# Kernel optimization log

Measured on AMD Instinct MI355X. Metric: run time of the kernel, lower is better.

Reference implementation:

```python
import jax, jax.numpy as jnp
import numpy as np


def setup_inputs() -> dict:
    key = jax.random.key(0)
    ks = jax.random.split(key, 4)
    d, d_k, d_v = 1024, 128, 128
    B, S = 4, 4096
    scale = 1.0 / np.sqrt(d)
    return {
        "X": jax.random.normal(ks[0], (B, S, d), dtype=jnp.float32),
        "W_q": jax.random.normal(ks[1], (d, d_k), dtype=jnp.float32) * scale,
        "b_q": jnp.zeros((d_k,), dtype=jnp.float32),
        "W_k": jax.random.normal(ks[2], (d, d_k), dtype=jnp.float32) * scale,
        "b_k": jnp.zeros((d_k,), dtype=jnp.float32),
        "W_v": jax.random.normal(ks[3], (d, d_v), dtype=jnp.float32) * scale,
        "b_v": jnp.zeros((d_v,), dtype=jnp.float32),
    }


def reference(X, W_q, b_q, W_k, b_k, W_v, b_v):
    # Projections: [B, S, d_k/d_v]
    Q = jnp.einsum("bsd,dk->bsk", X, W_q) + b_q
    K = jnp.einsum("bsd,dk->bsk", X, W_k) + b_k
    V = jnp.einsum("bsd,dv->bsv", X, W_v) + b_v

    d_k = Q.shape[-1]
    # Scaled dot-product scores: [B, S, S]
    scores = jnp.einsum("bqk,bsk->bqs", Q, K) / jnp.sqrt(jnp.float32(d_k))
    # Causal (lower-triangular) mask
    S = scores.shape[-1]
    causal = jnp.tril(jnp.ones((S, S), dtype=bool))
    scores = jnp.where(causal[None, :, :], scores, -jnp.inf)
    weights = jax.nn.softmax(scores, axis=-1)
    # Weighted sum of values: [B, S, d_v]
    return jnp.einsum("bqs,bsv->bqv", weights, V)
```

## Files before the change

### kernel.cpp

```cpp
#include <hip/hip_runtime.h>
#include <hip/hip_bf16.h>
#include <stdint.h>


typedef __bf16 bf16x8 __attribute__((ext_vector_type(8)));
typedef float  f32x4  __attribute__((ext_vector_type(4)));
typedef unsigned int u32x4 __attribute__((ext_vector_type(4)));
typedef unsigned int u32x2 __attribute__((ext_vector_type(2)));

using bf16 = __hip_bfloat16;

#define AS1 __attribute__((address_space(1)))
#define AS3 __attribute__((address_space(3)))

__device__ __forceinline__ void gl_lds16(const void* g, void* l) {
  __builtin_amdgcn_global_load_lds((AS1 uint32_t*)g, (AS3 uint32_t*)l, 16, 0, 0);
}

__global__ __launch_bounds__(256) void k_wt(const float* __restrict__ Wq,
                                            const float* __restrict__ Wk,
                                            const float* __restrict__ Wv,
                                            bf16* __restrict__ Wt) {
  __shared__ bf16 t[64][72];
  const float* W = blockIdx.z == 0 ? Wq : (blockIdx.z == 1 ? Wk : Wv);
  int k0 = blockIdx.x * 64, n0 = blockIdx.y * 64;
  int tid = threadIdx.x;
  int r = tid >> 4, c4 = (tid & 15) * 4;
#pragma unroll
  for (int s = 0; s < 4; ++s) {
    int rr = r + s * 16;
    float4 v = *(const float4*)(W + (size_t)(k0 + rr) * 128 + n0 + c4);
    t[rr][c4 + 0] = __float2bfloat16(v.x);
    t[rr][c4 + 1] = __float2bfloat16(v.y);
    t[rr][c4 + 2] = __float2bfloat16(v.z);
    t[rr][c4 + 3] = __float2bfloat16(v.w);
  }
  __syncthreads();
  bf16* out = Wt + (size_t)blockIdx.z * 128 * 1024;
#pragma unroll
  for (int s = 0; s < 4; ++s) {
    int rn = r + s * 16;
    union { bf16 h[4]; u32x2 v; } u;
    u.h[0] = t[c4 + 0][rn]; u.h[1] = t[c4 + 1][rn];
    u.h[2] = t[c4 + 2][rn]; u.h[3] = t[c4 + 3][rn];
    *(u32x2*)(out + (size_t)(n0 + rn) * 1024 + k0 + c4) = u.v;
  }
}

__global__ __launch_bounds__(512) void k_qkv(const float* __restrict__ X,
                                             const bf16* __restrict__ Wt,
                                             const float* __restrict__ bq,
                                             const float* __restrict__ bk,
                                             const float* __restrict__ bv,
                                             bf16* __restrict__ Qo,
                                             bf16* __restrict__ Ko,
                                             bf16* __restrict__ Vt) {
  __shared__ __align__(16) char smem[65536];
  float* Xs = (float*)smem;
  bf16* Ws = (bf16*)(smem + 16384);
  bf16* Vs = (bf16*)smem;

  const int m0 = blockIdx.x * 64;
  const int tid = threadIdx.x;
  const int lane = tid & 63;
  const int li = lane & 15, g = lane >> 4;
  const int wid = tid >> 6;
  const int wm = wid >> 2, wn = wid & 3;

  const int xr = tid >> 3;
  const int xc32 = (tid & 7) >> 1;
  const int xhf = tid & 1;
  const int wr = tid >> 2;
  const int wc = tid & 3;

  f32x4 acc[3][2][2] = {};

  {
    gl_lds16(X + (size_t)(m0 + xr) * 1024 + (xc32 ^ (xr & 3)) * 8 + xhf * 4,
             Xs + tid * 4);
#pragma unroll
    for (int z = 0; z < 3; ++z)
      gl_lds16(Wt + (size_t)z * 131072 + (size_t)wr * 1024 + (wc ^ (wr & 3)) * 8,
               Ws + z * 4096 + tid * 8);
  }
  int cur = 0;
  for (int kt = 0; kt < 32; ++kt) {
    __syncthreads();
    if (kt < 31) {
      const int k0 = (kt + 1) * 32;
      gl_lds16(X + (size_t)(m0 + xr) * 1024 + k0 + (xc32 ^ (xr & 3)) * 8 + xhf * 4,
               Xs + (cur ^ 1) * 2048 + tid * 4);
#pragma unroll
      for (int z = 0; z < 3; ++z)
        gl_lds16(Wt + (size_t)z * 131072 + (size_t)wr * 1024 + k0 + (wc ^ (wr & 3)) * 8,
                 Ws + (cur ^ 1) * 12288 + z * 4096 + tid * 8);
    }
    bf16x8 af[2];
#pragma unroll
    for (int mf = 0; mf < 2; ++mf) {
      int r = wm * 32 + mf * 16 + li;
      const float* xp = Xs + cur * 2048 + r * 32 + ((g ^ (r & 3)) * 8);
      f32x4 x0 = *(const f32x4*)xp;
      f32x4 x1 = *(const f32x4*)(xp + 4);
      union { bf16 h[8]; bf16x8 v; } u;
      u.h[0] = __float2bfloat16(x0[0]); u.h[1] = __float2bfloat16(x0[1]);
      u.h[2] = __float2bfloat16(x0[2]); u.h[3] = __float2bfloat16(x0[3]);
      u.h[4] = __float2bfloat16(x1[0]); u.h[5] = __float2bfloat16(x1[1]);
      u.h[6] = __float2bfloat16(x1[2]); u.h[7] = __float2bfloat16(x1[3]);
      af[mf] = u.v;
    }
#pragma unroll
    for (int z = 0; z < 3; ++z) {
#pragma unroll
      for (int nf = 0; nf < 2; ++nf) {
        int r = wn * 32 + nf * 16 + li;
        bf16x8 bfrag =
            *(const bf16x8*)(Ws + cur * 12288 + z * 4096 + r * 32 + ((g ^ (r & 3)) * 8));
#pragma unroll
        for (int mf = 0; mf < 2; ++mf)
          acc[z][mf][nf] = __builtin_amdgcn_mfma_f32_16x16x32_bf16(
              af[mf], bfrag, acc[z][mf][nf], 0, 0, 0);
      }
    }
    cur ^= 1;
  }

#pragma unroll
  for (int z = 0; z < 2; ++z) {
    const float* bias = z == 0 ? bq : bk;
    bf16* Out = z == 0 ? Qo : Ko;
    const float scale = z == 0 ? 0.12752404368678202f : 1.0f;
#pragma unroll
    for (int nf = 0; nf < 2; ++nf) {
      int col = wn * 32 + nf * 16 + li;
      float bb = bias[col];
#pragma unroll
      for (int mf = 0; mf < 2; ++mf)
#pragma unroll
        for (int j = 0; j < 4; ++j) {
          int row = m0 + wm * 32 + mf * 16 + g * 4 + j;
          Out[(size_t)row * 128 + col] =
              __float2bfloat16((acc[z][mf][nf][j] + bb) * scale);
        }
    }
  }

  __syncthreads();
#pragma unroll
  for (int nf = 0; nf < 2; ++nf) {
    int col = wn * 32 + nf * 16 + li;
    float bb = bv[col];
#pragma unroll
    for (int mf = 0; mf < 2; ++mf)
#pragma unroll
      for (int j = 0; j < 4; ++j) {
        int row = wm * 32 + mf * 16 + g * 4 + j;
        Vs[row * 136 + col] = __float2bfloat16(acc[2][mf][nf][j] + bb);
      }
  }
  __syncthreads();
  const int b = m0 >> 12;
  const int s_off = m0 & 4095;
#pragma unroll
  for (int t2 = 0; t2 < 2; ++t2) {
    int idx = tid + 512 * t2;
    int dv = idx & 127;
    int sg = idx >> 7;
    union { bf16 h[8]; u32x4 v; } u;
#pragma unroll
    for (int si = 0; si < 8; ++si) u.h[si] = Vs[(sg * 8 + si) * 136 + dv];
    *(u32x4*)(Vt + (size_t)(b * 128 + dv) * 4096 + s_off + sg * 8) = u.v;
  }
}

__global__ __launch_bounds__(512, 4) void k_attn(const bf16* __restrict__ Qb,
                                                 const bf16* __restrict__ Kb,
                                                 const bf16* __restrict__ Vt,
                                                 bf16* __restrict__ o_part,
                                                 float* __restrict__ l_part) {
  __shared__ __align__(16) bf16 Kls[2][64 * 128];
  __shared__ __align__(16) bf16 Vls[2][128 * 64];
  __shared__ __align__(16) bf16 Pls[8][16 * 36];

  const int bid = blockIdx.x;
  const int xcd = bid & 7;
  const int slot = xcd * 72 + (bid >> 3);
  const int b = slot / 144;
  const int s = 143 - (slot - b * 144);
  const int widx = b * 144 + s;
  int qt = 0;
#pragma unroll
  for (int q2 = 1; q2 < 32; ++q2) {
    int M = q2 >> 2;
    if ((M + 1) * (2 * M + (q2 & 3)) <= s) qt = q2;
  }
  const int Mq = qt >> 2;
  const int chunk = s - (Mq + 1) * (2 * Mq + (qt & 3));
  const int ntiles = 2 * qt + 2;
  const int nch = (qt + 4) >> 2;
  const int clen = ntiles / nch;
  const int crem = ntiles - clen * nch;
  const int kt0 = chunk * clen + min(chunk, crem);
  const int kt1 = kt0 + clen + (chunk < crem ? 1 : 0) - 1;

  const int tid = threadIdx.x;
  const int lane = tid & 63;
  const int li = lane & 15, g = lane >> 4;
  const int w8 = tid >> 6;

  bf16x8 qf[4];
#pragma unroll
  for (int ks = 0; ks < 4; ++ks)
    qf[ks] = *(const bf16x8*)(Qb +
        (size_t)(b * 4096 + qt * 128 + w8 * 16 + li) * 128 + ks * 32 + g * 8);

  f32x4 o[8] = {};
  f32x4 lacc = {};
  bf16x8 ones;
#pragma unroll
  for (int e = 0; e < 8; ++e) ones[e] = (__bf16)1.0f;

  bf16* P = &Pls[w8][0];
  const bf16* Vtb = Vt + (size_t)b * 128 * 4096;

  {
    const int kv0 = kt0 * 64;
#pragma unroll
    for (int ii = 0; ii < 2; ++ii) {
      int c = tid + 512 * ii;
      int r = c >> 4, cc = c & 15;
      gl_lds16(Kb + (size_t)(b * 4096 + kv0 + r) * 128 + (cc ^ (r & 7)) * 8,
               &Kls[0][c * 8]);
      int r2 = c >> 3, cc2 = c & 7;
      gl_lds16(Vtb + (size_t)r2 * 4096 + kv0 + (cc2 ^ (r2 & 7)) * 8,
               &Vls[0][c * 8]);
    }
  }
  int cur = 0;
  for (int kt = kt0; kt <= kt1; ++kt) {
    __syncthreads();
    if (kt < kt1) {
      const int kv0n = (kt + 1) * 64;
#pragma unroll
      for (int ii = 0; ii < 2; ++ii) {
        int c = tid + 512 * ii;
        int r = c >> 4, cc = c & 15;
        gl_lds16(Kb + (size_t)(b * 4096 + kv0n + r) * 128 + (cc ^ (r & 7)) * 8,
                 &Kls[cur ^ 1][c * 8]);
        int r2 = c >> 3, cc2 = c & 7;
        gl_lds16(Vtb + (size_t)r2 * 4096 + kv0n + (cc2 ^ (r2 & 7)) * 8,
                 &Vls[cur ^ 1][c * 8]);
      }
    }
    const bf16* Kl = &Kls[cur][0];
    const bf16* Vl = &Vls[cur][0];
    const int kv0 = kt * 64;

    f32x4 st[4] = {};
#pragma unroll
    for (int ks = 0; ks < 4; ++ks) {
      bf16x8 kf[4];
#pragma unroll
      for (int nf = 0; nf < 4; ++nf) {
        int r = nf * 16 + li;
        int ch = (ks * 4 + g) ^ (r & 7);
        kf[nf] = *(const bf16x8*)(Kl + r * 128 + ch * 8);
      }
#pragma unroll
      for (int nf = 0; nf < 4; ++nf)
        st[nf] = __builtin_amdgcn_mfma_f32_16x16x32_bf16(
            kf[nf], qf[ks], st[nf], 0, 0, 0);
    }

    if (kt >= 2 * qt) {
      const int dk = kv0 - qt * 128;
      const int qloc = w8 * 16 + li;
#pragma unroll
      for (int nf = 0; nf < 4; ++nf)
#pragma unroll
        for (int j = 0; j < 4; ++j)
          if (dk + nf * 16 + g * 4 + j > qloc) st[nf][j] = -1e30f;
    }

#pragma unroll
    for (int h = 0; h < 2; ++h) {
#pragma unroll
      for (int nfh = 0; nfh < 2; ++nfh) {
        const f32x4 sv = st[h * 2 + nfh];
        union { bf16 h4[4]; u32x2 v; } u;
#pragma unroll
        for (int j = 0; j < 4; ++j)
          u.h4[j] = __float2bfloat16(exp2f(sv[j]));
        *(u32x2*)(P + li * 36 + nfh * 16 + g * 4) = u.v;
      }
      bf16x8 pa = *(const bf16x8*)(P + li * 36 + g * 8);
#pragma unroll
      for (int dvf = 0; dvf < 8; ++dvf) {
        int r = dvf * 16 + li;
        int ch = (h * 4 + g) ^ (li & 7);
        bf16x8 vf = *(const bf16x8*)(Vl + r * 64 + ch * 8);
        o[dvf] = __builtin_amdgcn_mfma_f32_16x16x32_bf16(
            vf, pa, o[dvf], 0, 0, 0);
      }
      lacc = __builtin_amdgcn_mfma_f32_16x16x32_bf16(ones, pa, lacc, 0, 0, 0);
    }
    cur ^= 1;
  }

  bf16* op = o_part + (size_t)widx * (128 * 128);
  float* lp = l_part + widx * 128;
  {
    const int qloc = w8 * 16 + li;
    if (g == 0) lp[qloc] = lacc[0];
#pragma unroll
    for (int dvf = 0; dvf < 8; ++dvf) {
      union { bf16 h4[4]; u32x2 v; } u;
#pragma unroll
      for (int j = 0; j < 4; ++j) u.h4[j] = __float2bfloat16(o[dvf][j]);
      *(u32x2*)(op + (size_t)qloc * 128 + dvf * 16 + g * 4) = u.v;
    }
  }
}

__global__ __launch_bounds__(256) void k_comb(const bf16* __restrict__ op,
                                              const float* __restrict__ lp,
                                              float* __restrict__ out) {
  int i = blockIdx.x * 256 + threadIdx.x;
  int row = i >> 5;
  int col4 = (i & 31) * 4;
  int b = row >> 12;
  int rb = row & 4095;
  int qt = rb >> 7;
  int lr = rb & 127;
  int M = qt >> 2;
  int base = b * 144 + (M + 1) * (2 * M + (qt & 3));
  int n = (qt + 4) >> 2;
  float l = 0.0f;
  float acc0 = 0, acc1 = 0, acc2 = 0, acc3 = 0;
  for (int c = 0; c < n; ++c) {
    l += lp[(base + c) * 128 + lr];
    union { bf16 h[4]; u32x2 v; } u;
    u.v = *(const u32x2*)(op + (size_t)(base + c) * 16384 + lr * 128 + col4);
    acc0 += __bfloat162float(u.h[0]);
    acc1 += __bfloat162float(u.h[1]);
    acc2 += __bfloat162float(u.h[2]);
    acc3 += __bfloat162float(u.h[3]);
  }
  float linv = 1.0f / l;
  float4 rv;
  rv.x = acc0 * linv; rv.y = acc1 * linv; rv.z = acc2 * linv; rv.w = acc3 * linv;
  ((float4*)out)[i] = rv;
}

extern "C" void kernel_launch(void* const* d_in, const int* in_sizes, int n_in,
                              void* d_out, int out_size, void* d_ws, size_t ws_size,
                              hipStream_t stream) {
  const float* X  = (const float*)d_in[0];
  const float* Wq = (const float*)d_in[1];
  const float* bq = (const float*)d_in[2];
  const float* Wk = (const float*)d_in[3];
  const float* bk = (const float*)d_in[4];
  const float* Wv = (const float*)d_in[5];
  const float* bv = (const float*)d_in[6];
  float* out = (float*)d_out;

  char* ws = (char*)d_ws;
  bf16* Wt  = (bf16*)(ws + 0);
  bf16* Qb  = (bf16*)(ws + 786432);
  bf16* Kb  = (bf16*)(ws + 4980736);
  bf16* Vt  = (bf16*)(ws + 9175040);
  bf16* o_part = (bf16*)(ws + 13369344);
  float* l_part = (float*)(ws + 32243712);

  k_wt<<<dim3(16, 2, 3), dim3(256), 0, stream>>>(Wq, Wk, Wv, Wt);
  k_qkv<<<dim3(256), dim3(512), 0, stream>>>(X, Wt, bq, bk, bv, Qb, Kb, Vt);
  k_attn<<<dim3(576), dim3(512), 0, stream>>>(Qb, Kb, Vt, o_part, l_part);
  k_comb<<<dim3(2048), dim3(256), 0, stream>>>(o_part, l_part, out);
}
```

Baseline: 87.84 us.

## Use partial vmcnt waits with raw barriers for LDS prefetch; widen combine loads

In the QKV projection and attention loops, the full __syncthreads at the top of each iteration is replaced by an explicit s_waitcnt vmcnt(4) (or vmcnt(0) on the last iteration) plus raw s_barrier calls, with a second barrier after compute. Only the current tile's async global-to-LDS loads must finish before compute, so the next tile's prefetch stays in flight. The combine kernel now handles 8 columns per thread with 16-byte loads and runs half as many blocks. The hand-counted vmcnt depends on exactly four outstanding loads per thread and is fragile if the load count changes.

```diff
diff --git a/kernel.cpp b/kernel.cpp
--- a/kernel.cpp
+++ b/kernel.cpp
@@ -15,6 +15,15 @@
 
 __device__ __forceinline__ void gl_lds16(const void* g, void* l) {
   __builtin_amdgcn_global_load_lds((AS1 uint32_t*)g, (AS3 uint32_t*)l, 16, 0, 0);
+}
+
+__device__ __forceinline__ void wait_vm4() {
+  asm volatile("s_waitcnt vmcnt(4)" ::: "memory");
+  __builtin_amdgcn_sched_barrier(0);
+}
+__device__ __forceinline__ void wait_vm0() {
+  asm volatile("s_waitcnt vmcnt(0)" ::: "memory");
+  __builtin_amdgcn_sched_barrier(0);
 }
 
 __global__ __launch_bounds__(256) void k_wt(const float* __restrict__ Wq,
@@ -85,7 +94,6 @@
   }
   int cur = 0;
   for (int kt = 0; kt < 32; ++kt) {
-    __syncthreads();
     if (kt < 31) {
       const int k0 = (kt + 1) * 32;
       gl_lds16(X + (size_t)(m0 + xr) * 1024 + k0 + (xc32 ^ (xr & 3)) * 8 + xhf * 4,
@@ -94,7 +102,12 @@
       for (int z = 0; z < 3; ++z)
         gl_lds16(Wt + (size_t)z * 131072 + (size_t)wr * 1024 + k0 + (wc ^ (wr & 3)) * 8,
                  Ws + (cur ^ 1) * 12288 + z * 4096 + tid * 8);
-    }
+      wait_vm4();
+    } else {
+      wait_vm0();
+    }
+    __builtin_amdgcn_s_barrier();
+
     bf16x8 af[2];
 #pragma unroll
     for (int mf = 0; mf < 2; ++mf) {
@@ -122,6 +135,7 @@
               af[mf], bfrag, acc[z][mf][nf], 0, 0, 0);
       }
     }
+    __builtin_amdgcn_s_barrier();
     cur ^= 1;
   }
 
@@ -238,7 +252,6 @@
   }
   int cur = 0;
   for (int kt = kt0; kt <= kt1; ++kt) {
-    __syncthreads();
     if (kt < kt1) {
       const int kv0n = (kt + 1) * 64;
 #pragma unroll
@@ -251,7 +264,12 @@
         gl_lds16(Vtb + (size_t)r2 * 4096 + kv0n + (cc2 ^ (r2 & 7)) * 8,
                  &Vls[cur ^ 1][c * 8]);
       }
-    }
+      wait_vm4();
+    } else {
+      wait_vm0();
+    }
+    __builtin_amdgcn_s_barrier();
+
     const bf16* Kl = &Kls[cur][0];
     const bf16* Vl = &Vls[cur][0];
     const int kv0 = kt * 64;
@@ -304,6 +322,7 @@
       }
       lacc = __builtin_amdgcn_mfma_f32_16x16x32_bf16(ones, pa, lacc, 0, 0, 0);
     }
+    __builtin_amdgcn_s_barrier();
     cur ^= 1;
   }
 
@@ -326,8 +345,8 @@
                                               const float* __restrict__ lp,
                                               float* __restrict__ out) {
   int i = blockIdx.x * 256 + threadIdx.x;
-  int row = i >> 5;
-  int col4 = (i & 31) * 4;
+  int row = i >> 4;
+  int col8 = (i & 15) * 8;
   int b = row >> 12;
   int rb = row & 4095;
   int qt = rb >> 7;
@@ -336,20 +355,22 @@
   int base = b * 144 + (M + 1) * (2 * M + (qt & 3));
   int n = (qt + 4) >> 2;
   float l = 0.0f;
-  float acc0 = 0, acc1 = 0, acc2 = 0, acc3 = 0;
+  float acc[8] = {};
   for (int c = 0; c < n; ++c) {
     l += lp[(base + c) * 128 + lr];
-    union { bf16 h[4]; u32x2 v; } u;
-    u.v = *(const u32x2*)(op + (size_t)(base + c) * 16384 + lr * 128 + col4);
-    acc0 += __bfloat162float(u.h[0]);
-    acc1 += __bfloat162float(u.h[1]);
-    acc2 += __bfloat162float(u.h[2]);
-    acc3 += __bfloat162float(u.h[3]);
+    union { bf16 h[8]; u32x4 v; } u;
+    u.v = *(const u32x4*)(op + (size_t)(base + c) * 16384 + lr * 128 + col8);
+#pragma unroll
+    for (int j = 0; j < 8; ++j) acc[j] += __bfloat162float(u.h[j]);
   }
   float linv = 1.0f / l;
-  float4 rv;
-  rv.x = acc0 * linv; rv.y = acc1 * linv; rv.z = acc2 * linv; rv.w = acc3 * linv;
-  ((float4*)out)[i] = rv;
+  float4 r0, r1;
+  r0.x = acc[0] * linv; r0.y = acc[1] * linv;
+  r0.z = acc[2] * linv; r0.w = acc[3] * linv;
+  r1.x = acc[4] * linv; r1.y = acc[5] * linv;
+  r1.z = acc[6] * linv; r1.w = acc[7] * linv;
+  ((float4*)out)[i * 2] = r0;
+  ((float4*)out)[i * 2 + 1] = r1;
 }
 
 extern "C" void kernel_launch(void* const* d_in, const int* in_sizes, int n_in,
@@ -375,5 +396,5 @@
   k_wt<<<dim3(16, 2, 3), dim3(256), 0, stream>>>(Wq, Wk, Wv, Wt);
   k_qkv<<<dim3(256), dim3(512), 0, stream>>>(X, Wt, bq, bk, bv, Qb, Kb, Vt);
   k_attn<<<dim3(576), dim3(512), 0, stream>>>(Qb, Kb, Vt, o_part, l_part);
-  k_comb<<<dim3(2048), dim3(256), 0, stream>>>(o_part, l_part, out);
-}
+  k_comb<<<dim3(1024), dim3(256), 0, stream>>>(o_part, l_part, out);
+}
```

Result: faster. 85.05 us (-3.2%).
